# Kernel tuning notes

Hardware: AMD Instinct MI355X
Metric: run time of the kernel (lower is better)

The kernel has to match this reference:

```python
import jax, jax.numpy as jnp
from jax import lax
import numpy as np

LEAKY_SLOPE = 0.2  # tf.nn.leaky_relu default alpha


def _conv(x, w, b):
    # 3x3 SAME conv, NHWC / HWIO
    return lax.conv_general_dilated(x, w, (1, 1), 'SAME',
                                    dimension_numbers=('NHWC', 'HWIO', 'NHWC')) + b


def setup_inputs() -> dict:
    key = jax.random.key(0)
    ks = jax.random.split(key, 16)
    B, H, W, C = 4, 192, 640, 64
    sr = 2
    left = jax.random.normal(ks[0], (B, H, W, C), jnp.float32)
    right = jax.random.normal(ks[1], (B, H, W, C), jnp.float32)
    prev_disp = jax.random.uniform(ks[2], (B, H // 2, W // 2, 1), jnp.float32)
    # StereoEstimator conv stack: in = C + (2*sr+1) = 69
    chans = [C + (2 * sr + 1), 128, 128, 96, 64, 32, 1]
    inp = {'left': left, 'right': right, 'prev_disp': prev_disp, 'search_range': sr}
    for i in range(6):
        inp[f'w{i+1}'] = jax.random.normal(ks[3 + i], (3, 3, chans[i], chans[i + 1]), jnp.float32) * 0.05
        inp[f'b{i+1}'] = jnp.zeros((chans[i + 1],), jnp.float32)
    return inp


def _warp_right(right, disp):
    # disp: [B,H,W] horizontal displacement; sample right at x + disp (y unchanged).
    B, H, W, C = right.shape
    cx = jnp.arange(W, dtype=jnp.float32)[None, None, :] + disp  # [B,H,W]
    x0 = jnp.floor(cx)
    x1 = x0 + 1.0
    x_max = jnp.float32(W - 1)
    x0s = jnp.clip(x0, 0.0, x_max)
    x1s = jnp.clip(x1, 0.0, x_max)
    wt_x0 = (x1 - cx) * (x0 == x0s).astype(jnp.float32)
    wt_x1 = (cx - x0) * (x1 == x1s).astype(jnp.float32)
    i0 = x0s.astype(jnp.int32)[..., None]  # [B,H,W,1]
    i1 = x1s.astype(jnp.int32)[..., None]
    im00 = jnp.take_along_axis(right, i0, axis=2)
    im01 = jnp.take_along_axis(right, i1, axis=2)
    return wt_x0[..., None] * im00 + wt_x1[..., None] * im01


def _cost_volume(c1, warp, search_range):
    B, H, W, C = c1.shape
    padded = jnp.pad(warp, ((0, 0), (0, 0), (search_range, search_range), (0, 0)))
    costs = [jnp.mean(c1 * padded[:, :, i:W + i, :], axis=3)
             for i in range(2 * search_range + 1)]  # each [B,H,W]
    cost_vol = jnp.stack(costs, axis=3)  # [B,H,W,2sr+1]
    return jnp.concatenate([c1, cost_vol], axis=3)


def reference(left, right, prev_disp, search_range,
              w1, b1, w2, b2, w3, b3, w4, b4, w5, b5, w6, b6):
    B, H, W, C = left.shape
    # Resizing(bilinear) -> half-pixel bilinear resize, as tf.image.resize
    up = jax.image.resize(prev_disp, (B, H, W, 1), 'bilinear')
    disp = up[..., 0]
    warped = _warp_right(right, disp)
    costs = _cost_volume(left, warped, search_range)
    act = lambda x: jax.nn.leaky_relu(x, LEAKY_SLOPE)
    x = act(_conv(costs, w1, b1))
    x = act(_conv(x, w2, b2))
    x = act(_conv(x, w3, b3))
    x = act(_conv(x, w4, b4))
    x = act(_conv(x, w5, b5))
    x = _conv(x, w6, b6)  # linear
    return x
```

## Files before the change

kernel.cpp:

```cpp
#include <hip/hip_runtime.h>
#include <cstdint>
#include <cstddef>


#define LEAKY_SLOPE 0.2f

typedef float  f32x16 __attribute__((ext_vector_type(16)));
typedef short  s16x8  __attribute__((ext_vector_type(8)));
typedef short  s16x4  __attribute__((ext_vector_type(4)));

__device__ __forceinline__ unsigned short f2bf(float f) {
    unsigned u = __float_as_uint(f);
    u += 0x7FFFu + ((u >> 16) & 1u);
    return (unsigned short)(u >> 16);
}
__device__ __forceinline__ float bf2f(unsigned short s) {
    return __uint_as_float(((unsigned)s) << 16);
}
__device__ __forceinline__ float leaky(float v){ return v >= 0.f ? v : LEAKY_SLOPE * v; }

__global__ __launch_bounds__(256) void pack_weights(
    const float* __restrict__ src, short* __restrict__ dst,
    int CIN, int COUT, int KB, int NT, int total)
{
    int i = blockIdx.x * 256 + threadIdx.x;
    if (i >= total) return;
    int j    = i & 7;
    int lane = (i >> 3) & 63;
    int r    = i >> 9;
    int nt = r % NT; r /= NT;
    int kb = r % KB;
    int dydx = r / KB;
    int ci = kb * 16 + ((lane >> 5) << 3) + j;
    int co = nt * 32 + (lane & 31);
    float v = (ci < CIN) ? src[((size_t)dydx * CIN + ci) * COUT + co] : 0.f;
    dst[i] = (short)f2bf(v);
}

__global__ __launch_bounds__(256) void warp_costs_kernel(
    const float* __restrict__ left, const float* __restrict__ right,
    const float* __restrict__ prev, short* __restrict__ out,
    int H, int W)
{
    __shared__ float wt0s[68], wt1s[68];
    __shared__ int   i0s[68],  i1s[68];
    __shared__ __align__(16) short warp_s[68 * 72];
    __shared__ __align__(16) short left_s[64 * 72];

    const int tid = threadIdx.x;
    const int w0 = blockIdx.x * 64;
    const int hh = blockIdx.y % H;
    const int bb = blockIdx.y / H;
    const int H2 = H >> 1, W2 = W >> 1;

    if (tid < 68) {
        int w = w0 - 2 + tid;
        float sy = 0.5f * (float)hh - 0.25f;
        float sx = 0.5f * (float)w  - 0.25f;
        float y0f = floorf(sy), x0f = floorf(sx);
        float fy = sy - y0f, fx = sx - x0f;
        int y0 = (int)y0f, x0 = (int)x0f;
        int y0c = min(max(y0, 0), H2 - 1), y1c = min(max(y0 + 1, 0), H2 - 1);
        int x0c = min(max(x0, 0), W2 - 1), x1c = min(max(x0 + 1, 0), W2 - 1);
        const float* pb = prev + (size_t)bb * H2 * W2;
        float p00 = pb[y0c * W2 + x0c], p01 = pb[y0c * W2 + x1c];
        float p10 = pb[y1c * W2 + x0c], p11 = pb[y1c * W2 + x1c];
        float disp = (1.f - fy) * ((1.f - fx) * p00 + fx * p01)
                   + fy * ((1.f - fx) * p10 + fx * p11);
        float cx = (float)w + disp;
        float xf0 = floorf(cx), xf1 = xf0 + 1.f;
        float xmax = (float)(W - 1);
        float x0s = fminf(fmaxf(xf0, 0.f), xmax);
        float x1s = fminf(fmaxf(xf1, 0.f), xmax);
        wt0s[tid] = (xf1 - cx) * (xf0 == x0s ? 1.f : 0.f);
        wt1s[tid] = (cx - xf0) * (xf1 == x1s ? 1.f : 0.f);
        i0s[tid] = (int)x0s;
        i1s[tid] = (int)x1s;
    }
    __syncthreads();

    const float* rrow = right + (size_t)(bb * H + hh) * W * 64;
    const float* lrow = left  + (size_t)(bb * H + hh) * W * 64;
    const size_t obase = ((size_t)(bb * H + hh) * W + w0) * 96;

    for (int u = tid; u < 68 * 16; u += 256) {
        int px = u >> 4, c4 = (u & 15) * 4;
        float a = wt0s[px], b = wt1s[px];
        const float4 r0 = *(const float4*)(rrow + (size_t)i0s[px] * 64 + c4);
        const float4 r1 = *(const float4*)(rrow + (size_t)i1s[px] * 64 + c4);
        s16x4 o;
        o[0] = (short)f2bf(a * r0.x + b * r1.x);
        o[1] = (short)f2bf(a * r0.y + b * r1.y);
        o[2] = (short)f2bf(a * r0.z + b * r1.z);
        o[3] = (short)f2bf(a * r0.w + b * r1.w);
        *(s16x4*)(warp_s + px * 72 + c4) = o;
    }
    for (int u = tid; u < 64 * 16; u += 256) {
        int px = u >> 4, c4 = (u & 15) * 4;
        const float4 l = *(const float4*)(lrow + ((size_t)(w0 + px)) * 64 + c4);
        s16x4 o;
        o[0] = (short)f2bf(l.x);
        o[1] = (short)f2bf(l.y);
        o[2] = (short)f2bf(l.z);
        o[3] = (short)f2bf(l.w);
        *(s16x4*)(left_s + px * 72 + c4) = o;
        *(s16x4*)(out + obase + (size_t)px * 96 + c4) = o;
    }
    for (int u = tid; u < 64 * 3; u += 256) {
        int px = u / 3, c = 72 + (u % 3) * 8;
        s16x8 z = {0,0,0,0,0,0,0,0};
        *(s16x8*)(out + obase + (size_t)px * 96 + c) = z;
    }
    if (tid < 64) {
        out[obase + (size_t)tid * 96 + 69] = 0;
        out[obase + (size_t)tid * 96 + 70] = 0;
        out[obase + (size_t)tid * 96 + 71] = 0;
    }
    __syncthreads();

    for (int u = tid; u < 64 * 5; u += 256) {
        int px = u / 5, d = u - px * 5;
        int x = w0 + px + d - 2;
        float s = 0.f;
        if (x >= 0 && x < W) {
            const short* lp = left_s + px * 72;
            const short* wq = warp_s + (px + d) * 72;
#pragma unroll
            for (int c8 = 0; c8 < 8; ++c8) {
                s16x8 l8 = *(const s16x8*)(lp + c8 * 8);
                s16x8 w8 = *(const s16x8*)(wq + c8 * 8);
#pragma unroll
                for (int k = 0; k < 8; ++k)
                    s += bf2f((unsigned short)l8[k]) * bf2f((unsigned short)w8[k]);
            }
        }
        out[obase + (size_t)px * 96 + 64 + d] = (short)f2bf(s * (1.f / 64.f));
    }
}

template <int CINP, int COUT, bool RELU>
__global__ __launch_bounds__(256, 3) void conv_mfma(
    const short* __restrict__ in, const short* __restrict__ wp,
    const float* __restrict__ bias, short* __restrict__ out,
    int H, int W)
{
    constexpr int KB   = CINP / 16;
    constexpr int NT   = COUT / 32;
    constexpr int CIN8 = CINP / 8;
    constexpr int SL8  = (CINP == 96) ? 16 : CIN8;
    __shared__ __align__(16) short lds[132 * SL8 * 8];

    const int tid  = threadIdx.x;
    const int lane = tid & 63;
    const int wave = tid >> 6;
    const int l31  = lane & 31;
    const int lhi  = lane >> 5;
    const int w0 = blockIdx.x * 128;
    const int hh = blockIdx.y % H;
    const int bb = blockIdx.y / H;

    f32x16 acc[NT];
#pragma unroll
    for (int nt = 0; nt < NT; ++nt)
#pragma unroll
        for (int r = 0; r < 16; ++r) acc[nt][r] = 0.f;

    for (int dy = 0; dy < 3; ++dy) {
        __syncthreads();
        const int h = hh + dy - 1;
        const bool rowok = (h >= 0) && (h < H);
        const short* src = in + (size_t)(bb * H + h) * W * CINP;
        for (int u = tid; u < 130 * CIN8; u += 256) {
            int px = u / CIN8;
            int c8 = u - px * CIN8;
            int x = w0 - 1 + px;
            s16x8 v = {0,0,0,0,0,0,0,0};
            if (rowok && x >= 0 && x < W)
                v = *(const s16x8*)(src + (size_t)x * CINP + c8 * 8);
            *(s16x8*)(&lds[(px * SL8 + (c8 ^ (px & 7))) * 8]) = v;
        }
        __syncthreads();

#pragma unroll
        for (int dx = 0; dx < 3; ++dx) {
            const short* wdx = wp + (size_t)((dy * 3 + dx) * KB) * NT * 512;
            const int px = wave * 32 + l31 + dx;
            const int pxs = px * SL8;
            const int pxx = px & 7;
#pragma unroll 2
            for (int kb = 0; kb < KB; ++kb) {
                const int c8r = kb * 2 + lhi;
                s16x8 a = *(const s16x8*)(&lds[(pxs + (c8r ^ pxx)) * 8]);
                s16x8 b[NT];
#pragma unroll
                for (int nt = 0; nt < NT; ++nt)
                    b[nt] = *(const s16x8*)(wdx + ((size_t)(kb * NT + nt) * 64 + lane) * 8);
#pragma unroll
                for (int nt = 0; nt < NT; ++nt)
                    acc[nt] = __builtin_amdgcn_mfma_f32_32x32x16_bf16(
                        a, b[nt], acc[nt], 0, 0, 0);
            }
        }
    }

    const size_t rowbase = (size_t)(bb * H + hh) * W + w0;
    const int pxb = wave * 32 + 4 * lhi;
#pragma unroll
    for (int nt = 0; nt < NT; ++nt) {
        const int co = nt * 32 + l31;
        const float bv = bias[co];
#pragma unroll
        for (int r = 0; r < 16; ++r) {
            int px = pxb + (r & 3) + 8 * (r >> 2);
            float v = acc[nt][r] + bv;
            if (RELU) v = leaky(v);
            out[(rowbase + px) * COUT + co] = (short)f2bf(v);
        }
    }
}

__global__ __launch_bounds__(256) void conv_last_kernel(
    const short* __restrict__ in, const float* __restrict__ wgt,
    const float* __restrict__ bias, float* __restrict__ out,
    int H, int W, int npx)
{
    int idx = blockIdx.x * 256 + threadIdx.x;
    if (idx >= npx) return;
    int w = idx % W;
    int t = idx / W;
    int h = t % H;
    int b = t / H;

    float acc = bias[0];
#pragma unroll
    for (int dy = 0; dy < 3; ++dy) {
        int hy = h + dy - 1;
        if (hy < 0 || hy >= H) continue;
#pragma unroll
        for (int dx = 0; dx < 3; ++dx) {
            int x = w + dx - 1;
            if (x < 0 || x >= W) continue;
            const short* p = in + ((size_t)(b * H + hy) * W + x) * 32;
            const float* wk = wgt + (dy * 3 + dx) * 32;
#pragma unroll
            for (int c8 = 0; c8 < 4; ++c8) {
                s16x8 v = *(const s16x8*)(p + c8 * 8);
#pragma unroll
                for (int k = 0; k < 8; ++k)
                    acc += bf2f((unsigned short)v[k]) * wk[c8 * 8 + k];
            }
        }
    }
    out[idx] = acc;
}

extern "C" void kernel_launch(void* const* d_in, const int* in_sizes, int n_in,
                              void* d_out, int out_size, void* d_ws, size_t ws_size,
                              hipStream_t stream)
{
    constexpr int B = 4, H = 192, W = 640;
    constexpr int HW = H * W;

    const float* left  = (const float*)d_in[0];
    const float* right = (const float*)d_in[1];
    const float* prev  = (const float*)d_in[2];
    const float* w1 = (const float*)d_in[4];
    const float* b1 = (const float*)d_in[5];
    const float* w2 = (const float*)d_in[6];
    const float* b2 = (const float*)d_in[7];
    const float* w3 = (const float*)d_in[8];
    const float* b3 = (const float*)d_in[9];
    const float* w4 = (const float*)d_in[10];
    const float* b4 = (const float*)d_in[11];
    const float* w5 = (const float*)d_in[12];
    const float* b5 = (const float*)d_in[13];
    const float* w6 = (const float*)d_in[14];
    const float* b6 = (const float*)d_in[15];
    float* out = (float*)d_out;

    constexpr int S1 = 9 * 6 * 4 * 512;
    constexpr int S2 = 9 * 8 * 4 * 512;
    constexpr int S3 = 9 * 8 * 3 * 512;
    constexpr int S4 = 9 * 6 * 2 * 512;
    constexpr int S5 = 9 * 4 * 1 * 512;
    constexpr int P1 = 0, P2 = P1 + S1, P3 = P2 + S2, P4 = P3 + S3, P5 = P4 + S4;
    constexpr size_t WPAD = 524288;

    short* wsS = (short*)d_ws;
    pack_weights<<<(S1 + 255) / 256, 256, 0, stream>>>(w1, wsS + P1,  69, 128, 6, 4, S1);
    pack_weights<<<(S2 + 255) / 256, 256, 0, stream>>>(w2, wsS + P2, 128, 128, 8, 4, S2);
    pack_weights<<<(S3 + 255) / 256, 256, 0, stream>>>(w3, wsS + P3, 128,  96, 8, 3, S3);
    pack_weights<<<(S4 + 255) / 256, 256, 0, stream>>>(w4, wsS + P4,  96,  64, 6, 2, S4);
    pack_weights<<<(S5 + 255) / 256, 256, 0, stream>>>(w5, wsS + P5,  64,  32, 4, 1, S5);

    auto need = [&](int nb) -> size_t {
        return (WPAD + 2ull * nb * HW * 128) * sizeof(short);
    };
    int nb = 1;
    if (ws_size >= need(4)) nb = 4;
    else if (ws_size >= need(2)) nb = 2;

    const int H2 = H / 2, W2 = W / 2;

    for (int b0 = 0; b0 < B; b0 += nb) {
        const int npx = nb * HW;
        short* X = wsS + WPAD;
        short* Y = X + (size_t)nb * HW * 128;

        const float* leftb  = left  + (size_t)b0 * HW * 64;
        const float* rightb = right + (size_t)b0 * HW * 64;
        const float* prevb  = prev  + (size_t)b0 * H2 * W2;
        float* outb = out + (size_t)b0 * HW;

        warp_costs_kernel<<<dim3(W / 64, nb * H), 256, 0, stream>>>(
            leftb, rightb, prevb, X, H, W);

        conv_mfma< 96, 128, true><<<dim3(W / 128, nb * H), 256, 0, stream>>>(
            X, wsS + P1, b1, Y, H, W);
        conv_mfma<128, 128, true><<<dim3(W / 128, nb * H), 256, 0, stream>>>(
            Y, wsS + P2, b2, X, H, W);
        conv_mfma<128,  96, true><<<dim3(W / 128, nb * H), 256, 0, stream>>>(
            X, wsS + P3, b3, Y, H, W);
        conv_mfma< 96,  64, true><<<dim3(W / 128, nb * H), 256, 0, stream>>>(
            Y, wsS + P4, b4, X, H, W);
        conv_mfma< 64,  32, true><<<dim3(W / 128, nb * H), 256, 0, stream>>>(
            X, wsS + P5, b5, Y, H, W);

        conv_last_kernel<<<(npx + 255) / 256, 256, 0, stream>>>(
            Y, w6, b6, outb, H, W, npx);
    }
}
```

Measured before the change: 1.093 ms.

## Split conv MFMA work across waves in a 2D pixel-by-channel grid

Each block's waves are now arranged as WM x WN. Waves split the output-channel tiles (WN=2 when NT>=2), and each wave covers several 32-pixel M tiles, so each loaded weight fragment feeds several MFMAs. This cuts global weight loads per MFMA, which previously went to every wave, at the cost of more LDS A-fragment reads and more accumulator registers. The last 64->32 layer now uses 128-thread blocks, with two waves each covering two pixel tiles.

```diff
diff --git a/kernel.cpp b/kernel.cpp
--- a/kernel.cpp
+++ b/kernel.cpp
@@ -138,8 +138,8 @@
     }
 }
 
-template <int CINP, int COUT, bool RELU>
-__global__ __launch_bounds__(256, 3) void conv_mfma(
+template <int CINP, int COUT, int TPB, bool RELU>
+__global__ __launch_bounds__(TPB, 3) void conv_mfma(
     const short* __restrict__ in, const short* __restrict__ wp,
     const float* __restrict__ bias, short* __restrict__ out,
     int H, int W)
@@ -148,29 +148,37 @@
     constexpr int NT   = COUT / 32;
     constexpr int CIN8 = CINP / 8;
     constexpr int SL8  = (CINP == 96) ? 16 : CIN8;
+    constexpr int WN   = (NT >= 2) ? 2 : 1;
+    constexpr int WM   = (TPB / 64) / WN;
+    constexpr int MT   = 4 / WM;
+    constexpr int NTW  = (NT + WN - 1) / WN;
     __shared__ __align__(16) short lds[132 * SL8 * 8];
 
     const int tid  = threadIdx.x;
     const int lane = tid & 63;
     const int wave = tid >> 6;
+    const int wn   = wave % WN;
+    const int wm   = wave / WN;
     const int l31  = lane & 31;
     const int lhi  = lane >> 5;
     const int w0 = blockIdx.x * 128;
     const int hh = blockIdx.y % H;
     const int bb = blockIdx.y / H;
 
-    f32x16 acc[NT];
-#pragma unroll
-    for (int nt = 0; nt < NT; ++nt)
-#pragma unroll
-        for (int r = 0; r < 16; ++r) acc[nt][r] = 0.f;
+    f32x16 acc[MT][NTW];
+#pragma unroll
+    for (int mt = 0; mt < MT; ++mt)
+#pragma unroll
+        for (int j = 0; j < NTW; ++j)
+#pragma unroll
+            for (int r = 0; r < 16; ++r) acc[mt][j][r] = 0.f;
 
     for (int dy = 0; dy < 3; ++dy) {
         __syncthreads();
         const int h = hh + dy - 1;
         const bool rowok = (h >= 0) && (h < H);
         const short* src = in + (size_t)(bb * H + h) * W * CINP;
-        for (int u = tid; u < 130 * CIN8; u += 256) {
+        for (int u = tid; u < 130 * CIN8; u += TPB) {
             int px = u / CIN8;
             int c8 = u - px * CIN8;
             int x = w0 - 1 + px;
@@ -184,37 +192,51 @@
 #pragma unroll
         for (int dx = 0; dx < 3; ++dx) {
             const short* wdx = wp + (size_t)((dy * 3 + dx) * KB) * NT * 512;
-            const int px = wave * 32 + l31 + dx;
-            const int pxs = px * SL8;
-            const int pxx = px & 7;
 #pragma unroll 2
             for (int kb = 0; kb < KB; ++kb) {
                 const int c8r = kb * 2 + lhi;
-                s16x8 a = *(const s16x8*)(&lds[(pxs + (c8r ^ pxx)) * 8]);
-                s16x8 b[NT];
-#pragma unroll
-                for (int nt = 0; nt < NT; ++nt)
-                    b[nt] = *(const s16x8*)(wdx + ((size_t)(kb * NT + nt) * 64 + lane) * 8);
-#pragma unroll
-                for (int nt = 0; nt < NT; ++nt)
-                    acc[nt] = __builtin_amdgcn_mfma_f32_32x32x16_bf16(
-                        a, b[nt], acc[nt], 0, 0, 0);
+                s16x8 a[MT];
+#pragma unroll
+                for (int mt = 0; mt < MT; ++mt) {
+                    const int px = (wm * MT + mt) * 32 + l31 + dx;
+                    a[mt] = *(const s16x8*)(&lds[(px * SL8 + (c8r ^ (px & 7))) * 8]);
+                }
+                s16x8 b[NTW];
+#pragma unroll
+                for (int j = 0; j < NTW; ++j) {
+                    const int tile = wn * NTW + j;
+                    if (tile < NT)
+                        b[j] = *(const s16x8*)(wdx + ((size_t)(kb * NT + tile) * 64 + lane) * 8);
+                }
+#pragma unroll
+                for (int j = 0; j < NTW; ++j) {
+                    if (wn * NTW + j >= NT) continue;
+#pragma unroll
+                    for (int mt = 0; mt < MT; ++mt)
+                        acc[mt][j] = __builtin_amdgcn_mfma_f32_32x32x16_bf16(
+                            a[mt], b[j], acc[mt][j], 0, 0, 0);
+                }
             }
         }
     }
 
     const size_t rowbase = (size_t)(bb * H + hh) * W + w0;
-    const int pxb = wave * 32 + 4 * lhi;
-#pragma unroll
-    for (int nt = 0; nt < NT; ++nt) {
-        const int co = nt * 32 + l31;
+#pragma unroll
+    for (int j = 0; j < NTW; ++j) {
+        const int tile = wn * NTW + j;
+        if (tile >= NT) continue;
+        const int co = tile * 32 + l31;
         const float bv = bias[co];
 #pragma unroll
-        for (int r = 0; r < 16; ++r) {
-            int px = pxb + (r & 3) + 8 * (r >> 2);
-            float v = acc[nt][r] + bv;
-            if (RELU) v = leaky(v);
-            out[(rowbase + px) * COUT + co] = (short)f2bf(v);
+        for (int mt = 0; mt < MT; ++mt) {
+            const int pxb = (wm * MT + mt) * 32 + 4 * lhi;
+#pragma unroll
+            for (int r = 0; r < 16; ++r) {
+                int px = pxb + (r & 3) + 8 * (r >> 2);
+                float v = acc[mt][j][r] + bv;
+                if (RELU) v = leaky(v);
+                out[(rowbase + px) * COUT + co] = (short)f2bf(v);
+            }
         }
     }
 }
@@ -315,15 +337,15 @@
         warp_costs_kernel<<<dim3(W / 64, nb * H), 256, 0, stream>>>(
             leftb, rightb, prevb, X, H, W);
 
-        conv_mfma< 96, 128, true><<<dim3(W / 128, nb * H), 256, 0, stream>>>(
+        conv_mfma< 96, 128, 256, true><<<dim3(W / 128, nb * H), 256, 0, stream>>>(
             X, wsS + P1, b1, Y, H, W);
-        conv_mfma<128, 128, true><<<dim3(W / 128, nb * H), 256, 0, stream>>>(
+        conv_mfma<128, 128, 256, true><<<dim3(W / 128, nb * H), 256, 0, stream>>>(
             Y, wsS + P2, b2, X, H, W);
-        conv_mfma<128,  96, true><<<dim3(W / 128, nb * H), 256, 0, stream>>>(
+        conv_mfma<128,  96, 256, true><<<dim3(W / 128, nb * H), 256, 0, stream>>>(
             X, wsS + P3, b3, Y, H, W);
-        conv_mfma< 96,  64, true><<<dim3(W / 128, nb * H), 256, 0, stream>>>(
+        conv_mfma< 96,  64, 256, true><<<dim3(W / 128, nb * H), 256, 0, stream>>>(
             Y, wsS + P4, b4, X, H, W);
-        conv_mfma< 64,  32, true><<<dim3(W / 128, nb * H), 256, 0, stream>>>(
+        conv_mfma< 64,  32, 128, true><<<dim3(W / 128, nb * H), 128, 0, stream>>>(
             X, wsS + P5, b5, Y, H, W);
 
         conv_last_kernel<<<(npx + 255) / 256, 256, 0, stream>>>(
```

New measurement: 1.009 ms. 7.7% less time.
